# Kernel tuning notes

Hardware: AMD Instinct MI355X
Metric: run time of the kernel (lower is better)

The kernel has to match this reference:

```python
import jax, jax.numpy as jnp
import numpy as np

DK = 8.0          # sqrt(in_dim) with in_dim = 64
BN_SCALE = 1.0 / np.float32(np.sqrt(1.0 + 1e-5))  # eval-mode BatchNorm3d at init (mean=0, var=1, gamma=1, beta=0)


def conv3d(x, w, b):
    # x: [B,Cin,D1,D2,D3], w: [Cout,Cin,3,3,3], stride 1, padding 1 == SAME
    y = jax.lax.conv_general_dilated(
        x, w, window_strides=(1, 1, 1), padding='SAME',
        dimension_numbers=('NCDHW', 'OIDHW', 'NCDHW'))
    return y + b[None, :, None, None, None]


def axial(qm, km, vm):
    # qm/km/vm: [B,C,S,L,M]; attention over L with keys along M-contraction.
    # scores[b,c,s,i,j] = sum_m (q/dk)[...,i,m] * k[...,j,m]  -> [B,C,S,L,L]
    s = jnp.einsum('bcsim,bcsjm->bcsij', qm / DK, km)
    # torch nn.Softmax(dim=1) applied to [N,L,L] normalizes over the FIRST L axis (i)
    a = jax.nn.softmax(s, axis=-2)
    return jnp.einsum('bcsij,bcsjm->bcsim', a, vm)


def setup_inputs() -> dict:
    key = jax.random.key(0)
    ks = jax.random.split(key, 5)
    B, C, H, W, D = 2, 64, 64, 64, 64
    x = jax.random.normal(ks[0], (B, C, H, W, D), jnp.float32)
    Wq = jax.random.normal(ks[1], (C, C, 3, 3, 3), jnp.float32) * 0.02
    Wk = jax.random.normal(ks[2], (C, C, 3, 3, 3), jnp.float32) * 0.02
    Wv = jax.random.normal(ks[3], (C, C, 3, 3, 3), jnp.float32) * 0.02
    Wc = jax.random.normal(ks[4], (C, 3 * C, 3, 3, 3), jnp.float32) * 0.02
    z = jnp.zeros((C,), jnp.float32)
    return {"x": x, "Wq": Wq, "bq": z, "Wk": Wk, "bk": z,
            "Wv": Wv, "bv": z, "Wc": Wc, "bc": z}


def reference(x, Wq, bq, Wk, bk, Wv, bv, Wc, bc):
    # projections (dropout is inactive at inference)
    q = conv3d(x, Wq, bq)
    k = conv3d(x, Wk, bk)
    v = conv3d(x, Wv, bv)
    P = jnp.transpose

    # ---- loop over D slices: attend over H (and over W in the transposed pass) ----
    pa = (0, 1, 4, 2, 3)        # [B,C,D,H,W]
    ava = axial(P(q, pa), P(k, pa), P(v, pa))          # [B,C,D,H,W]
    ava = P(ava, (0, 1, 3, 4, 2))                       # -> [B,C,H,W,D]
    pb = (0, 1, 4, 3, 2)        # [B,C,D,W,H]
    ava1 = axial(P(q, pb), P(k, pb), P(v, pb))          # [B,C,D,W,H]
    ava1 = P(ava1, (0, 1, 4, 3, 2))                     # -> [B,C,H,W,D]
    AVa = (ava + ava1) * 0.5

    # ---- loop over W slices: attend over H (and over D) ----
    pc = (0, 1, 3, 2, 4)        # [B,C,W,H,D]
    avb = axial(P(q, pc), P(k, pc), P(v, pc))           # [B,C,W,H,D]
    avb = P(avb, (0, 1, 3, 2, 4))                       # -> [B,C,H,W,D]
    pd = (0, 1, 3, 4, 2)        # [B,C,W,D,H]
    avb1 = axial(P(q, pd), P(k, pd), P(v, pd))          # [B,C,W,D,H]
    avb1 = P(avb1, (0, 1, 4, 2, 3))                     # -> [B,C,H,W,D]
    AVb = (avb + avb1) * 0.5

    # ---- loop over H slices: attend over W (and over D) ----
    avc = axial(q, k, v)                                 # [B,C,H,W,D]
    pe = (0, 1, 2, 4, 3)        # [B,C,H,D,W]
    avc1 = axial(P(q, pe), P(k, pe), P(v, pe))          # [B,C,H,D,W]
    avc1 = P(avc1, (0, 1, 2, 4, 3))                     # -> [B,C,H,W,D]
    AVc = (avc + avc1) * 0.5

    cat = jnp.concatenate([AVa, AVb, AVc], axis=1)      # [B,3C,H,W,D]
    y = jax.nn.relu(conv3d(cat, Wc, bc) * BN_SCALE)     # Conv_3x3x3: conv + BN(eval) + ReLU
    y = y * BN_SCALE                                    # outer BatchNorm3d (eval)
    return y + q
```

## Files before the change

### kernel.cpp

```cpp
#include <hip/hip_runtime.h>

typedef unsigned short u16;
typedef unsigned int u32;
typedef __attribute__((ext_vector_type(8))) __bf16 bf16x8;
typedef __attribute__((ext_vector_type(4))) float f32x4;
typedef __attribute__((ext_vector_type(4))) u16 u16x4;

#define VOL 262144

__device__ __forceinline__ u16 f2bf(float f) {
  u32 u = __builtin_bit_cast(u32, f);
  u32 r = u + 0x7FFFu + ((u >> 16) & 1u);
  return (u16)(r >> 16);
}
__device__ __forceinline__ float bf2f(u16 h) {
  return __builtin_bit_cast(float, ((u32)h) << 16);
}
__device__ __forceinline__ bf16x8 ldsfrag(const u16* p) { return *(const bf16x8*)p; }

__device__ __forceinline__ int swA(int row, int col) {
  return row * 64 + (col ^ (((row ^ (row >> 3)) & 7) << 3));
}
__device__ __forceinline__ int colS96(int dpos, int col) {
  int s = ((dpos >> 1) ^ (dpos >> 3)) & 7;
  int b = (col >> 3) + s;
  if (b >= 12) b -= 12;
  return (b << 3) | (col & 7);
}

__global__ __launch_bounds__(256) void swz_qkv(const float* __restrict__ Wq,
    const float* __restrict__ Wk, const float* __restrict__ Wv, u16* __restrict__ out) {
  int idx = blockIdx.x * 256 + threadIdx.x;
  if (idx >= 54 * 12 * 64 * 8) return;
  int jj = idx & 7;
  int lane = (idx >> 3) & 63;
  int t = idx >> 9;
  int nf = t % 12, s = t / 12;
  int dh = s / 18, sub = s % 18;
  int dw = sub / 6, dd = (sub >> 1) % 3, c32 = sub & 1;
  int coutg = nf * 16 + (lane & 15);
  int cin = c32 * 32 + (lane >> 4) * 8 + jj;
  const float* W = (coutg < 64) ? Wq : ((coutg < 128) ? Wk : Wv);
  int c = coutg & 63;
  out[idx] = f2bf(W[(c * 64 + cin) * 27 + dh * 9 + dw * 3 + dd]);
}

__global__ __launch_bounds__(256) void swz_c(const float* __restrict__ Wc, u16* __restrict__ out) {
  int idx = blockIdx.x * 256 + threadIdx.x;
  if (idx >= 162 * 4 * 64 * 8) return;
  int jj = idx & 7;
  int lane = (idx >> 3) & 63;
  int nf = (idx >> 9) & 3;
  int s = idx >> 11;
  int dh = s / 54, rem = s % 54;
  int hf = rem / 27, sub = rem % 27;
  int dw = sub / 9, dd = (sub / 3) % 3, c32 = sub % 3;
  int cout = nf * 16 + (lane & 15);
  int cin = hf * 96 + c32 * 32 + (lane >> 4) * 8 + jj;
  out[idx] = f2bf(Wc[(cout * 192 + cin) * 27 + dh * 9 + dw * 3 + dd]);
}

__global__ __launch_bounds__(512, 2) void conv_qkv(const float* __restrict__ x,
    const u16* __restrict__ BQ, const float* __restrict__ bq, const float* __restrict__ bk,
    const float* __restrict__ bv, u16* __restrict__ qb, u16* __restrict__ kb,
    u16* __restrict__ vb) {
  __shared__ __align__(16) u16 xT[4 * 66 * 72];
  int tid = threadIdx.x;
  int id = blockIdx.x;
  int lin = (id & 7) * 512 + (id >> 3);
  int b = lin >> 11, h = (lin >> 5) & 63, w0 = (lin & 31) * 2;
  int wave = tid >> 6, lane = tid & 63, r = lane & 15, g = lane >> 4;
  int mhalf = wave >> 2, nq = wave & 3;
  int pairid = tid >> 3, seg = tid & 7;
  if (tid < 256) {
    int wwi = tid >> 6, ci = tid & 63;
    xT[(wwi * 66 + 0) * 72 + ci] = 0;
    xT[(wwi * 66 + 65) * 72 + ci] = 0;
  }
  f32x4 acc[4][3];
#pragma unroll
  for (int i = 0; i < 4; ++i)
#pragma unroll
    for (int j = 0; j < 3; ++j)
#pragma unroll
      for (int e = 0; e < 4; ++e) acc[i][j][e] = 0.0f;

  for (int dh = 0; dh < 3; ++dh) {
    int hh = h + dh - 1;
    if ((unsigned)hh >= 64u) continue;
    __syncthreads();
#pragma unroll
    for (int pi = 0; pi < 2; ++pi) {
      int pair = pairid + 64 * pi;
      int wwi = pair >> 5, cin0 = (pair & 31) * 2;
      int ww = w0 + wwi - 1;
      float4 a0{}, a1{}, b0{}, b1{};
      if ((unsigned)ww < 64u) {
        const float* p = x + (size_t)(b * 64 + cin0) * VOL + hh * 4096 + ww * 64 + seg * 8;
        a0 = *(const float4*)p;        a1 = *(const float4*)(p + 4);
        b0 = *(const float4*)(p + VOL); b1 = *(const float4*)(p + VOL + 4);
      }
      u16 ua[8], ub[8];
      ua[0]=f2bf(a0.x); ua[1]=f2bf(a0.y); ua[2]=f2bf(a0.z); ua[3]=f2bf(a0.w);
      ua[4]=f2bf(a1.x); ua[5]=f2bf(a1.y); ua[6]=f2bf(a1.z); ua[7]=f2bf(a1.w);
      ub[0]=f2bf(b0.x); ub[1]=f2bf(b0.y); ub[2]=f2bf(b0.z); ub[3]=f2bf(b0.w);
      ub[4]=f2bf(b1.x); ub[5]=f2bf(b1.y); ub[6]=f2bf(b1.z); ub[7]=f2bf(b1.w);
      int rowb = wwi * 66;
#pragma unroll
      for (int di = 0; di < 8; ++di) {
        int dpos = seg * 8 + di + 1;
        *(u32*)&xT[(rowb + dpos) * 72 + (cin0 ^ (((dpos >> 3) & 7) << 3))] =
            (u32)ua[di] | ((u32)ub[di] << 16);
      }
    }
    __syncthreads();
    for (int sub = 0; sub < 18; ++sub) {
      int s = dh * 18 + sub;
      int dw = sub / 6, dd = (sub >> 1) % 3, c32 = sub & 1;
      int colb = c32 * 32 + g * 8;
      int wwi = mhalf + dw;
      bf16x8 A[4];
#pragma unroll
      for (int l = 0; l < 4; ++l) {
        int dpos = l * 16 + r + dd;
        A[l] = ldsfrag(&xT[(wwi * 66 + dpos) * 72 + (colb ^ (((dpos >> 3) & 7) << 3))]);
      }
      const u16* Bp = BQ + ((size_t)(s * 12 + nq * 3) * 64 + lane) * 8;
#pragma unroll
      for (int nf = 0; nf < 3; ++nf) {
        bf16x8 Bf = *(const bf16x8*)(Bp + nf * 512);
#pragma unroll
        for (int l = 0; l < 4; ++l)
          acc[l][nf] = __builtin_amdgcn_mfma_f32_16x16x32_bf16(A[l], Bf, acc[l][nf], 0, 0, 0);
      }
    }
  }
#pragma unroll
  for (int nf = 0; nf < 3; ++nf) {
    int coutg = (nq * 3 + nf) * 16 + r;
    int ten = coutg >> 6, c = coutg & 63;
    u16* dst = (ten == 0) ? qb : ((ten == 1) ? kb : vb);
    const float* bias = (ten == 0) ? bq : ((ten == 1) ? bk : bv);
    float bsv = bias[c];
#pragma unroll
    for (int l = 0; l < 4; ++l) {
      int d0 = l * 16 + g * 4;
      int idx = (b * 64 + c) * VOL + h * 4096 + (w0 + mhalf) * 64 + d0;
      u16x4 o;
#pragma unroll
      for (int jj = 0; jj < 4; ++jj) o[jj] = f2bf(acc[l][nf][jj] + bsv);
      *(u16x4*)(dst + idx) = o;
    }
  }
}

__global__ __launch_bounds__(256, 6) void ktranspose(const u16* __restrict__ src,
    u16* __restrict__ dst, int P, int Q) {
  __shared__ __align__(16) u16 tile[64 * 72];
  int tid = threadIdx.x;
  int id = blockIdx.x;
  int bc = id >> 6, t = id & 63;
  int qt = Q >> 6;
  int p0 = (t / qt) * 64, q0 = (t % qt) * 64;
  const u16* s = src + (size_t)bc * VOL;
  u16* d = dst + (size_t)bc * VOL;
#pragma unroll
  for (int it = 0; it < 2; ++it) {
    int c = tid + 256 * it;
    int i2 = c >> 3, sg = c & 7;
    *(uint4*)&tile[i2 * 72 + ((sg * 8) ^ (((i2 >> 3) & 7) << 3))] =
        *(const uint4*)&s[(size_t)(p0 + i2) * Q + q0 + sg * 8];
  }
  __syncthreads();
  int j = tid >> 2, ms = tid & 3;
  u16 vals[16];
#pragma unroll
  for (int ii = 0; ii < 16; ++ii) {
    int row = ms * 16 + ii;
    vals[ii] = tile[row * 72 + (j ^ (((row >> 3) & 7) << 3))];
  }
  uint4 o0, o1;
  o0.x = (u32)vals[0] | ((u32)vals[1] << 16);
  o0.y = (u32)vals[2] | ((u32)vals[3] << 16);
  o0.z = (u32)vals[4] | ((u32)vals[5] << 16);
  o0.w = (u32)vals[6] | ((u32)vals[7] << 16);
  o1.x = (u32)vals[8] | ((u32)vals[9] << 16);
  o1.y = (u32)vals[10] | ((u32)vals[11] << 16);
  o1.z = (u32)vals[12] | ((u32)vals[13] << 16);
  o1.w = (u32)vals[14] | ((u32)vals[15] << 16);
  size_t drow = (size_t)(q0 + j) * P + p0 + ms * 16;
  *(uint4*)&d[drow] = o0;
  *(uint4*)&d[drow + 8] = o1;
}

__global__ __launch_bounds__(256, 2) void attn_pair(const u16* __restrict__ q,
    const u16* __restrict__ k, const u16* __restrict__ v, u16* __restrict__ dst,
    int uStride, int sMul) {
  __shared__ __align__(16) u16 sm[6 * 4096];
  u16* LQ = sm;             u16* LK = sm + 4096;      u16* LV = sm + 2 * 4096;
  u16* LQT = sm + 3 * 4096; u16* LKT = sm + 4 * 4096; u16* LVT = sm + 5 * 4096;
  u16* A1 = LK;
  u16* A2 = LKT;
  int tid = threadIdx.x;
  int id = blockIdx.x;
  int bc = id >> 6, sidx = id & 63;
  size_t base = (size_t)bc * VOL + (size_t)sidx * sMul;
  int wave = tid >> 6, lane = tid & 63, r = lane & 15, g = lane >> 4;
  int pairid = tid >> 3, seg = tid & 7;
  int u0 = pairid * 2;
  const u16* srcs[3] = {q, k, v};
  u16* Ln_[3] = {LQ, LK, LV};
  u16* Lt_[3] = {LQT, LKT, LVT};
#pragma unroll
  for (int t3 = 0; t3 < 3; ++t3) {
    const u16* p = srcs[t3] + base + (size_t)u0 * uStride + seg * 8;
    uint4 ra = *(const uint4*)p;
    uint4 rb = *(const uint4*)(p + uStride);
    *(uint4*)&Ln_[t3][swA(u0, seg * 8)] = ra;
    *(uint4*)&Ln_[t3][swA(u0 + 1, seg * 8)] = rb;
    union { uint4 vv; u16 ss[8]; } Ua, Ub;
    Ua.vv = ra; Ub.vv = rb;
#pragma unroll
    for (int vi = 0; vi < 8; ++vi) {
      int vvx = seg * 8 + vi;
      *(u32*)&Lt_[t3][swA(vvx, u0)] = (u32)Ua.ss[vi] | ((u32)Ub.ss[vi] << 16);
    }
  }
  __syncthreads();
  int row0 = wave * 16;
  f32x4 s1[4], s2[4];
#pragma unroll
  for (int nf = 0; nf < 4; ++nf)
#pragma unroll
    for (int e = 0; e < 4; ++e) { s1[nf][e] = 0.f; s2[nf][e] = 0.f; }
#pragma unroll
  for (int ks = 0; ks < 2; ++ks) {
    int cb = ks * 32 + g * 8;
    bf16x8 aK = ldsfrag(&LK[swA(row0 + r, cb)]);
    bf16x8 aKT = ldsfrag(&LKT[swA(row0 + r, cb)]);
#pragma unroll
    for (int nf = 0; nf < 4; ++nf) {
      bf16x8 bQ = ldsfrag(&LQ[swA(nf * 16 + r, cb)]);
      bf16x8 bQT = ldsfrag(&LQT[swA(nf * 16 + r, cb)]);
      s1[nf] = __builtin_amdgcn_mfma_f32_16x16x32_bf16(aK, bQ, s1[nf], 0, 0, 0);
      s2[nf] = __builtin_amdgcn_mfma_f32_16x16x32_bf16(aKT, bQT, s2[nf], 0, 0, 0);
    }
  }
  __syncthreads();
#pragma unroll
  for (int m2 = 0; m2 < 2; ++m2) {
    f32x4* ss = m2 ? s2 : s1;
    u16* Adst = m2 ? A2 : A1;
#pragma unroll
    for (int jj = 0; jj < 4; ++jj) {
      float mx = fmaxf(fmaxf(ss[0][jj], ss[1][jj]), fmaxf(ss[2][jj], ss[3][jj]));
      mx = fmaxf(mx, __shfl_xor(mx, 1, 64));
      mx = fmaxf(mx, __shfl_xor(mx, 2, 64));
      mx = fmaxf(mx, __shfl_xor(mx, 4, 64));
      mx = fmaxf(mx, __shfl_xor(mx, 8, 64));
      float p0 = __expf((ss[0][jj] - mx) * 0.125f);
      float p1 = __expf((ss[1][jj] - mx) * 0.125f);
      float p2 = __expf((ss[2][jj] - mx) * 0.125f);
      float p3 = __expf((ss[3][jj] - mx) * 0.125f);
      float sum = p0 + p1 + p2 + p3;
      sum += __shfl_xor(sum, 1, 64);
      sum += __shfl_xor(sum, 2, 64);
      sum += __shfl_xor(sum, 4, 64);
      sum += __shfl_xor(sum, 8, 64);
      float inv = 1.0f / sum;
      ss[0][jj] = p0 * inv; ss[1][jj] = p1 * inv; ss[2][jj] = p2 * inv; ss[3][jj] = p3 * inv;
    }
    int j0 = row0 + g * 4;
#pragma unroll
    for (int nf = 0; nf < 4; ++nf) {
      int i = nf * 16 + r;
      int a0 = swA(i, j0);
      *(u32*)&Adst[a0]     = (u32)f2bf(ss[nf][0]) | ((u32)f2bf(ss[nf][1]) << 16);
      *(u32*)&Adst[a0 + 2] = (u32)f2bf(ss[nf][2]) | ((u32)f2bf(ss[nf][3]) << 16);
    }
  }
  __syncthreads();
  f32x4 o[4];
#pragma unroll
  for (int nf = 0; nf < 4; ++nf)
#pragma unroll
    for (int e = 0; e < 4; ++e) o[nf][e] = 0.f;
#pragma unroll
  for (int ks = 0; ks < 2; ++ks) {
    int cb = ks * 32 + g * 8;
    bf16x8 aA = ldsfrag(&A1[swA(row0 + r, cb)]);
    bf16x8 aV = ldsfrag(&LV[swA(row0 + r, cb)]);
#pragma unroll
    for (int nf = 0; nf < 4; ++nf) {
      bf16x8 bVT = ldsfrag(&LVT[swA(nf * 16 + r, cb)]);
      bf16x8 bA2 = ldsfrag(&A2[swA(nf * 16 + r, cb)]);
      o[nf] = __builtin_amdgcn_mfma_f32_16x16x32_bf16(aA, bVT, o[nf], 0, 0, 0);
      o[nf] = __builtin_amdgcn_mfma_f32_16x16x32_bf16(aV, bA2, o[nf], 0, 0, 0);
    }
  }
#pragma unroll
  for (int nf = 0; nf < 4; ++nf) {
    int vv = nf * 16 + r;
#pragma unroll
    for (int jj = 0; jj < 4; ++jj) {
      int u = row0 + g * 4 + jj;
      dst[base + (size_t)u * uStride + vv] = f2bf(o[nf][jj] * 0.5f);
    }
  }
}

__global__ __launch_bounds__(512, 2) void conv_final(const u16* __restrict__ AVa,
    const u16* __restrict__ AVb, const u16* __restrict__ AVc, const u16* __restrict__ BCw,
    const float* __restrict__ bcb, const u16* __restrict__ qb, float* __restrict__ out) {
  __shared__ __align__(16) u16 xT[6 * 66 * 96];
  int tid = threadIdx.x;
  int id = blockIdx.x;
  int lin = (id & 7) * 256 + (id >> 3);
  int b = lin >> 10, h = (lin >> 4) & 63, w0 = (lin & 15) * 4;
  int wave = tid >> 6, lane = tid & 63, r = lane & 15, g = lane >> 4;
  int mw = wave >> 1, nw = wave & 1;
  int pairid = tid >> 3, seg = tid & 7;
  for (int z = tid; z < 576; z += 512) {
    int wwi = z / 96, ci = z % 96;
    xT[(wwi * 66 + 0) * 96 + ci] = 0;
    xT[(wwi * 66 + 65) * 96 + ci] = 0;
  }
  f32x4 acc[4][2];
#pragma unroll
  for (int i = 0; i < 4; ++i)
#pragma unroll
    for (int j = 0; j < 2; ++j)
#pragma unroll
      for (int e = 0; e < 4; ++e) acc[i][j][e] = 0.f;

  for (int dh = 0; dh < 3; ++dh) {
    int hh = h + dh - 1;
    if ((unsigned)hh >= 64u) continue;
    for (int hf = 0; hf < 2; ++hf) {
      __syncthreads();
#pragma unroll
      for (int pi = 0; pi < 5; ++pi) {
        int pair = pairid + 64 * pi;
        if (pair < 288) {
          int wwi = pair / 48;
          int cp = (pair % 48) * 2;
          int cing = hf * 96 + cp;
          int ten = cing >> 6, c = cing & 63;
          const u16* sp = (ten == 0) ? AVa : ((ten == 1) ? AVb : AVc);
          int ww = w0 + wwi - 1;
          uint4 ra{}, rb{};
          if ((unsigned)ww < 64u) {
            const u16* p = sp + (size_t)(b * 64 + c) * VOL + hh * 4096 + ww * 64 + seg * 8;
            ra = *(const uint4*)p;
            rb = *(const uint4*)(p + VOL);
          }
          union { uint4 vv; u16 ss[8]; } Ua, Ub;
          Ua.vv = ra; Ub.vv = rb;
          int rowb = wwi * 66;
#pragma unroll
          for (int di = 0; di < 8; ++di) {
            int dpos = seg * 8 + di + 1;
            *(u32*)&xT[(rowb + dpos) * 96 + colS96(dpos, cp)] =
                (u32)Ua.ss[di] | ((u32)Ub.ss[di] << 16);
          }
        }
      }
      __syncthreads();
      for (int sub = 0; sub < 27; ++sub) {
        int s = dh * 54 + hf * 27 + sub;
        int dw = sub / 9, dd = (sub / 3) % 3, c32 = sub % 3;
        int colb = c32 * 32 + g * 8;
        int wwi = mw + dw;
        bf16x8 A[4];
#pragma unroll
        for (int dq = 0; dq < 4; ++dq) {
          int dpos = dq * 16 + r + dd;
          A[dq] = ldsfrag(&xT[(wwi * 66 + dpos) * 96 + colS96(dpos, colb)]);
        }
        const u16* Bp = BCw + ((size_t)(s * 4 + nw * 2) * 64 + lane) * 8;
#pragma unroll
        for (int nf = 0; nf < 2; ++nf) {
          bf16x8 Bf = *(const bf16x8*)(Bp + nf * 512);
#pragma unroll
          for (int dq = 0; dq < 4; ++dq)
            acc[dq][nf] = __builtin_amdgcn_mfma_f32_16x16x32_bf16(A[dq], Bf, acc[dq][nf], 0, 0, 0);
        }
      }
    }
  }
  const float S = 0.9999950000374997f;
#pragma unroll
  for (int nf = 0; nf < 2; ++nf) {
    int cout = (nw * 2 + nf) * 16 + r;
    float bsv = bcb[cout];
#pragma unroll
    for (int dq = 0; dq < 4; ++dq) {
      int d0 = dq * 16 + g * 4;
      int idx = (b * 64 + cout) * VOL + h * 4096 + (w0 + mw) * 64 + d0;
      u16x4 qv = *(const u16x4*)(qb + idx);
      float4 ov;
      float t0 = (acc[dq][nf][0] + bsv) * S; t0 = t0 > 0.f ? t0 : 0.f; ov.x = t0 * S + bf2f(qv[0]);
      float t1 = (acc[dq][nf][1] + bsv) * S; t1 = t1 > 0.f ? t1 : 0.f; ov.y = t1 * S + bf2f(qv[1]);
      float t2 = (acc[dq][nf][2] + bsv) * S; t2 = t2 > 0.f ? t2 : 0.f; ov.z = t2 * S + bf2f(qv[2]);
      float t3 = (acc[dq][nf][3] + bsv) * S; t3 = t3 > 0.f ? t3 : 0.f; ov.w = t3 * S + bf2f(qv[3]);
      *(float4*)(out + idx) = ov;
    }
  }
}

extern "C" void kernel_launch(void* const* d_in, const int* in_sizes, int n_in,
                              void* d_out, int out_size, void* d_ws, size_t ws_size,
                              hipStream_t stream) {
  const float* x  = (const float*)d_in[0];
  const float* Wq = (const float*)d_in[1];
  const float* bq = (const float*)d_in[2];
  const float* Wk = (const float*)d_in[3];
  const float* bk = (const float*)d_in[4];
  const float* Wv = (const float*)d_in[5];
  const float* bv = (const float*)d_in[6];
  const float* Wc = (const float*)d_in[7];
  const float* bc = (const float*)d_in[8];
  float* out = (float*)d_out;
  u16* ws = (u16*)d_ws;
  const size_t T = (size_t)33554432;
  u16* qb = ws;
  u16* kb = ws + T;
  u16* vb = ws + 2 * T;
  u16* qT = ws + 3 * T;
  u16* kT = ws + 4 * T;
  u16* vT = ws + 5 * T;
  u16* avaT = ws + 6 * T;
  u16* BQ = ws + 7 * T;
  u16* BC = BQ + 331776;
  u16* AVa = qT;
  u16* AVb = kT;
  u16* AVc = vT;

  swz_qkv<<<1296, 256, 0, stream>>>(Wq, Wk, Wv, BQ);
  swz_c<<<1296, 256, 0, stream>>>(Wc, BC);
  conv_qkv<<<4096, 512, 0, stream>>>(x, BQ, bq, bk, bv, qb, kb, vb);
  ktranspose<<<8192, 256, 0, stream>>>(qb, qT, 4096, 64);
  ktranspose<<<8192, 256, 0, stream>>>(kb, kT, 4096, 64);
  ktranspose<<<8192, 256, 0, stream>>>(vb, vT, 4096, 64);
  attn_pair<<<8192, 256, 0, stream>>>(qT, kT, vT, avaT, 64, 4096);
  ktranspose<<<8192, 256, 0, stream>>>(avaT, AVa, 64, 4096);
  attn_pair<<<8192, 256, 0, stream>>>(qb, kb, vb, AVb, 4096, 64);
  attn_pair<<<8192, 256, 0, stream>>>(qb, kb, vb, AVc, 64, 4096);
  conv_final<<<2048, 512, 0, stream>>>(AVa, AVb, AVc, BC, bc, qb, out);
}
```

Baseline: 1.087 ms.

## Stage final conv input per tensor in 64-channel chunks with XOR swizzle

The final conv now stages its 192 input channels as three 64-channel chunks, one per attention tensor, instead of two 96-channel halves. This shrinks shared memory per block and replaces the modular colS96 swizzle with the cheaper XOR swizzle used in the QKV conv. It also drops the per-pair tensor selection branches and fully unrolls the inner MFMA loops in both convs, with the weight pre-swizzle reordered to match. The cost is one extra barrier-separated staging phase per dh step.

New measurement: 1.528 ms. 40.5% more time.

```diff
diff --git a/kernel.cpp b/kernel.cpp
--- a/kernel.cpp
+++ b/kernel.cpp
@@ -20,12 +20,6 @@
 
 __device__ __forceinline__ int swA(int row, int col) {
   return row * 64 + (col ^ (((row ^ (row >> 3)) & 7) << 3));
-}
-__device__ __forceinline__ int colS96(int dpos, int col) {
-  int s = ((dpos >> 1) ^ (dpos >> 3)) & 7;
-  int b = (col >> 3) + s;
-  if (b >= 12) b -= 12;
-  return (b << 3) | (col & 7);
 }
 
 __global__ __launch_bounds__(256) void swz_qkv(const float* __restrict__ Wq,
@@ -53,10 +47,10 @@
   int nf = (idx >> 9) & 3;
   int s = idx >> 11;
   int dh = s / 54, rem = s % 54;
-  int hf = rem / 27, sub = rem % 27;
-  int dw = sub / 9, dd = (sub / 3) % 3, c32 = sub % 3;
+  int t = rem / 18, sub = rem % 18;
+  int dw = sub / 6, dd = (sub >> 1) % 3, c32 = sub & 1;
   int cout = nf * 16 + (lane & 15);
-  int cin = hf * 96 + c32 * 32 + (lane >> 4) * 8 + jj;
+  int cin = t * 64 + c32 * 32 + (lane >> 4) * 8 + jj;
   out[idx] = f2bf(Wc[(cout * 192 + cin) * 27 + dh * 9 + dw * 3 + dd]);
 }
 
@@ -114,8 +108,8 @@
       }
     }
     __syncthreads();
+#pragma unroll
     for (int sub = 0; sub < 18; ++sub) {
-      int s = dh * 18 + sub;
       int dw = sub / 6, dd = (sub >> 1) % 3, c32 = sub & 1;
       int colb = c32 * 32 + g * 8;
       int wwi = mhalf + dw;
@@ -125,7 +119,7 @@
         int dpos = l * 16 + r + dd;
         A[l] = ldsfrag(&xT[(wwi * 66 + dpos) * 72 + (colb ^ (((dpos >> 3) & 7) << 3))]);
       }
-      const u16* Bp = BQ + ((size_t)(s * 12 + nq * 3) * 64 + lane) * 8;
+      const u16* Bp = BQ + ((size_t)((dh * 18 + sub) * 12 + nq * 3) * 64 + lane) * 8;
 #pragma unroll
       for (int nf = 0; nf < 3; ++nf) {
         bf16x8 Bf = *(const bf16x8*)(Bp + nf * 512);
@@ -312,7 +306,7 @@
 __global__ __launch_bounds__(512, 2) void conv_final(const u16* __restrict__ AVa,
     const u16* __restrict__ AVb, const u16* __restrict__ AVc, const u16* __restrict__ BCw,
     const float* __restrict__ bcb, const u16* __restrict__ qb, float* __restrict__ out) {
-  __shared__ __align__(16) u16 xT[6 * 66 * 96];
+  __shared__ __align__(16) u16 xT[6 * 66 * 72];
   int tid = threadIdx.x;
   int id = blockIdx.x;
   int lin = (id & 7) * 256 + (id >> 3);
@@ -320,10 +314,10 @@
   int wave = tid >> 6, lane = tid & 63, r = lane & 15, g = lane >> 4;
   int mw = wave >> 1, nw = wave & 1;
   int pairid = tid >> 3, seg = tid & 7;
-  for (int z = tid; z < 576; z += 512) {
-    int wwi = z / 96, ci = z % 96;
-    xT[(wwi * 66 + 0) * 96 + ci] = 0;
-    xT[(wwi * 66 + 65) * 96 + ci] = 0;
+  if (tid < 384) {
+    int wwi = tid >> 6, ci = tid & 63;
+    xT[(wwi * 66 + 0) * 72 + ci] = 0;
+    xT[(wwi * 66 + 65) * 72 + ci] = 0;
   }
   f32x4 acc[4][2];
 #pragma unroll
@@ -336,48 +330,43 @@
   for (int dh = 0; dh < 3; ++dh) {
     int hh = h + dh - 1;
     if ((unsigned)hh >= 64u) continue;
-    for (int hf = 0; hf < 2; ++hf) {
+    for (int t = 0; t < 3; ++t) {
+      const u16* sp = (t == 0) ? AVa : ((t == 1) ? AVb : AVc);
       __syncthreads();
 #pragma unroll
-      for (int pi = 0; pi < 5; ++pi) {
+      for (int pi = 0; pi < 3; ++pi) {
         int pair = pairid + 64 * pi;
-        if (pair < 288) {
-          int wwi = pair / 48;
-          int cp = (pair % 48) * 2;
-          int cing = hf * 96 + cp;
-          int ten = cing >> 6, c = cing & 63;
-          const u16* sp = (ten == 0) ? AVa : ((ten == 1) ? AVb : AVc);
-          int ww = w0 + wwi - 1;
-          uint4 ra{}, rb{};
-          if ((unsigned)ww < 64u) {
-            const u16* p = sp + (size_t)(b * 64 + c) * VOL + hh * 4096 + ww * 64 + seg * 8;
-            ra = *(const uint4*)p;
-            rb = *(const uint4*)(p + VOL);
-          }
-          union { uint4 vv; u16 ss[8]; } Ua, Ub;
-          Ua.vv = ra; Ub.vv = rb;
-          int rowb = wwi * 66;
-#pragma unroll
-          for (int di = 0; di < 8; ++di) {
-            int dpos = seg * 8 + di + 1;
-            *(u32*)&xT[(rowb + dpos) * 96 + colS96(dpos, cp)] =
-                (u32)Ua.ss[di] | ((u32)Ub.ss[di] << 16);
-          }
+        int wwi = pair >> 5, cin0 = (pair & 31) * 2;
+        int ww = w0 + wwi - 1;
+        uint4 ra{}, rb{};
+        if ((unsigned)ww < 64u) {
+          const u16* p = sp + (size_t)(b * 64 + cin0) * VOL + hh * 4096 + ww * 64 + seg * 8;
+          ra = *(const uint4*)p;
+          rb = *(const uint4*)(p + VOL);
         }
+        union { uint4 vv; u16 ss[8]; } Ua, Ub;
+        Ua.vv = ra; Ub.vv = rb;
+        int rowb = wwi * 66;
+#pragma unroll
+        for (int di = 0; di < 8; ++di) {
+          int dpos = seg * 8 + di + 1;
+          *(u32*)&xT[(rowb + dpos) * 72 + (cin0 ^ (((dpos >> 3) & 7) << 3))] =
+              (u32)Ua.ss[di] | ((u32)Ub.ss[di] << 16);
+        }
       }
       __syncthreads();
-      for (int sub = 0; sub < 27; ++sub) {
-        int s = dh * 54 + hf * 27 + sub;
-        int dw = sub / 9, dd = (sub / 3) % 3, c32 = sub % 3;
+#pragma unroll
+      for (int sub = 0; sub < 18; ++sub) {
+        int dw = sub / 6, dd = (sub >> 1) % 3, c32 = sub & 1;
         int colb = c32 * 32 + g * 8;
         int wwi = mw + dw;
         bf16x8 A[4];
 #pragma unroll
         for (int dq = 0; dq < 4; ++dq) {
           int dpos = dq * 16 + r + dd;
-          A[dq] = ldsfrag(&xT[(wwi * 66 + dpos) * 96 + colS96(dpos, colb)]);
+          A[dq] = ldsfrag(&xT[(wwi * 66 + dpos) * 72 + (colb ^ (((dpos >> 3) & 7) << 3))]);
         }
-        const u16* Bp = BCw + ((size_t)(s * 4 + nw * 2) * 64 + lane) * 8;
+        const u16* Bp = BCw + ((size_t)((((dh * 3 + t) * 18 + sub) * 4) + nw * 2) * 64 + lane) * 8;
 #pragma unroll
         for (int nf = 0; nf < 2; ++nf) {
           bf16x8 Bf = *(const bf16x8*)(Bp + nf * 512);
```
